# Optimization experiments

Hardware: AMD Instinct MI355X
Metric: run time of the kernel (lower is better)

## Reference

```python
import jax, jax.numpy as jnp
import numpy as np

B, S, D_MODEL, H, D_KV, D_FF = 2, 2048, 1024, 16, 64, 4096
NUM_BUCKETS, MAX_DISTANCE = 32, 128
EPS = 1e-6


def rms_norm(x, w, eps=EPS):
    var = jnp.mean(jnp.square(x), axis=-1, keepdims=True)
    return x * jax.lax.rsqrt(var + eps) * w


def gelu_new(x):
    c = np.sqrt(2.0 / np.pi).astype(np.float32)
    return 0.5 * x * (1.0 + jnp.tanh(c * (x + 0.044715 * x * x * x)))


def rel_position_bucket(qlen, klen, num_buckets=NUM_BUCKETS, max_distance=MAX_DISTANCE):
    # bidirectional (encoder) T5 bucketing
    ctx = jnp.arange(qlen)[:, None]
    mem = jnp.arange(klen)[None, :]
    rel = mem - ctx  # [q, k]
    nb = num_buckets // 2
    ret = (rel > 0).astype(jnp.int32) * nb
    n = jnp.abs(rel)
    max_exact = nb // 2
    is_small = n < max_exact
    val_large = max_exact + (
        jnp.log(jnp.maximum(n, 1).astype(jnp.float32) / max_exact)
        / np.log(max_distance / max_exact) * (nb - max_exact)
    ).astype(jnp.int32)
    val_large = jnp.minimum(val_large, nb - 1)
    return ret + jnp.where(is_small, n, val_large)


def setup_inputs() -> dict:
    key = jax.random.key(0)
    ks = jax.random.split(key, 12)
    sd = 1.0 / np.sqrt(D_MODEL)
    sf = 1.0 / np.sqrt(D_FF)
    return {
        "hidden_states": jax.random.normal(ks[0], (B, S, D_MODEL), jnp.float32),
        "attention_mask": jnp.ones((B, S), jnp.float32),
        "ln1_w": jnp.ones((D_MODEL,), jnp.float32),
        "wq": jax.random.normal(ks[1], (D_MODEL, H * D_KV), jnp.float32) * sd,
        "wk": jax.random.normal(ks[2], (D_MODEL, H * D_KV), jnp.float32) * sd,
        "wv": jax.random.normal(ks[3], (D_MODEL, H * D_KV), jnp.float32) * sd,
        "rel_bias": jax.random.normal(ks[4], (NUM_BUCKETS, H), jnp.float32) * 0.5,
        "wo": jax.random.normal(ks[5], (H * D_KV, D_MODEL), jnp.float32) * sd,
        "ln2_w": jnp.ones((D_MODEL,), jnp.float32),
        "w1": jax.random.normal(ks[6], (D_MODEL, D_FF), jnp.float32) * sd,
        "w2": jax.random.normal(ks[7], (D_MODEL, D_FF), jnp.float32) * sd,
        "w_out": jax.random.normal(ks[8], (D_FF, D_MODEL), jnp.float32) * sf,
    }


def reference(hidden_states, attention_mask, ln1_w, wq, wk, wv, rel_bias, wo,
              ln2_w, w1, w2, w_out):
    b, s, _ = hidden_states.shape
    # --- self attention (pre-LN) ---
    normed = rms_norm(hidden_states, ln1_w)
    q = (normed @ wq).reshape(b, s, H, D_KV)
    k = (normed @ wk).reshape(b, s, H, D_KV)
    v = (normed @ wv).reshape(b, s, H, D_KV)
    scores = jnp.einsum('bqhd,bkhd->bhqk', q, k)  # no 1/sqrt(d) scaling (T5)
    buckets = rel_position_bucket(s, s)            # [q, k] int32
    bias = rel_bias[buckets]                       # [q, k, H]
    scores = scores + jnp.transpose(bias, (2, 0, 1))[None]
    mask_add = (1.0 - attention_mask)[:, None, None, :] * -10000.0
    probs = jax.nn.softmax(scores + mask_add, axis=-1)
    ctx = jnp.einsum('bhqk,bkhd->bqhd', probs, v).reshape(b, s, H * D_KV)
    hidden = hidden_states + ctx @ wo
    # --- gated FFN (pre-LN) ---
    normed2 = rms_norm(hidden, ln2_w)
    ff = (gelu_new(normed2 @ w1) * (normed2 @ w2)) @ w_out
    return hidden + ff
```

## Files before the change

### kernel.cpp

```cpp
#include <hip/hip_runtime.h>
#include <math.h>

typedef unsigned short u16;
typedef unsigned int u32;
typedef __attribute__((ext_vector_type(8))) short short8;
typedef __attribute__((ext_vector_type(4))) float f32x4;

__device__ __forceinline__ float b2f(u16 u) {
    u32 x = ((u32)u) << 16;
    return __builtin_bit_cast(float, x);
}
__device__ __forceinline__ u16 f2b(float f) {
    u32 x = __builtin_bit_cast(u32, f);
    u32 r = x + 0x7fffu + ((x >> 16) & 1u);
    return (u16)(r >> 16);
}
__device__ __forceinline__ void split_hl(float x, u16& h, u16& l) {
    u16 hb = f2b(x);
    h = hb;
    l = f2b(x - b2f(hb));
}
__device__ __forceinline__ float gelu_new_f(float x) {
    const float c = 0.7978845608028654f;
    float y = c * (x + 0.044715f * x * x * x);
    float t = 1.0f - 2.0f / (1.0f + __expf(2.0f * y));
    return 0.5f * x * (1.0f + t);
}
__device__ __forceinline__ float scrub(float v, float s) {
    return (fabsf(v) < 1e25f) ? v : s;
}
__device__ __forceinline__ void gld16(const void* g, void* l) {
    __builtin_amdgcn_global_load_lds((const __attribute__((address_space(1))) u32*)g,
                                     (__attribute__((address_space(3))) u32*)l,
                                     16, 0, 0);
}
__device__ __forceinline__ short8 ldf(const u16* p) { return *(const short8*)p; }

__global__ __launch_bounds__(256) void transpose_cvt(const float* __restrict__ src,
                                                     u16* __restrict__ dst, int R, int C) {
    __shared__ u16 t[32][33];
    int c0 = blockIdx.x * 32, r0 = blockIdx.y * 32;
    int x = threadIdx.x & 31, y = threadIdx.x >> 5;
#pragma unroll
    for (int i = 0; i < 32; i += 8)
        t[y + i][x] = f2b(src[(size_t)(r0 + y + i) * C + c0 + x]);
    __syncthreads();
#pragma unroll
    for (int i = 0; i < 32; i += 8)
        dst[(size_t)(c0 + y + i) * R + r0 + x] = t[x][y + i];
}

__global__ void bias_table_kernel(const float* __restrict__ rel_bias,
                                  const float* __restrict__ mask,
                                  float* __restrict__ tab,
                                  float* __restrict__ mask_add) {
    int idx = blockIdx.x * 256 + threadIdx.x;
    if (idx < 4095) {
        int rel = idx - 2047;
        int ret = rel > 0 ? 16 : 0;
        int n = rel < 0 ? -rel : rel;
        int bucket;
        if (n < 8) {
            bucket = ret + n;
        } else {
            int v = 8 + (int)(logf((float)n * 0.125f) * (8.0f / 2.7725887222397811f));
            v = v < 15 ? v : 15;
            bucket = ret + v;
        }
#pragma unroll
        for (int h = 0; h < 16; h++)
            tab[h * 4096 + idx] = rel_bias[bucket * 16 + h];
    }
    if (idx < 4096)
        mask_add[idx] = (1.0f - mask[idx]) * -10000.0f - 20.0f;
}

__global__ __launch_bounds__(256) void rmsnorm_k(const float* __restrict__ X,
                                                 const float* __restrict__ W,
                                                 u16* __restrict__ Y) {
    __shared__ float red[4];
    int row = blockIdx.x, tid = threadIdx.x;
    const float* xr = X + (size_t)row * 1024;
    float4 x = *(const float4*)(xr + tid * 4);
    float ss = x.x * x.x + x.y * x.y + x.z * x.z + x.w * x.w;
#pragma unroll
    for (int off = 32; off; off >>= 1) ss += __shfl_xor(ss, off, 64);
    if ((tid & 63) == 0) red[tid >> 6] = ss;
    __syncthreads();
    float tot = red[0] + red[1] + red[2] + red[3];
    float s = rsqrtf(tot * (1.0f / 1024.0f) + 1e-6f);
    float4 w4 = *(const float4*)(W + tid * 4);
    float y0 = scrub(x.x * s * w4.x, 1e3f);
    float y1 = scrub(x.y * s * w4.y, 1e3f);
    float y2 = scrub(x.z * s * w4.z, 1e3f);
    float y3 = scrub(x.w * s * w4.w, 1e3f);
    uint2 o;
    o.x = (u32)f2b(y0) | ((u32)f2b(y1) << 16);
    o.y = (u32)f2b(y2) | ((u32)f2b(y3) << 16);
    *(uint2*)(Y + (size_t)row * 1024 + tid * 4) = o;
}


__global__ __launch_bounds__(256) void gemm_qkv(const u16* __restrict__ A,
                                                const u16* __restrict__ Bt,
                                                float* __restrict__ qb,
                                                u16* __restrict__ Kh,
                                                u16* __restrict__ Kl,
                                                u16* __restrict__ vT) {
    const int K = 1024;
    __shared__ __align__(16) u16 As[128 * 64];
    __shared__ __align__(16) u16 Bs[128 * 64];
    int tid = threadIdx.x;
    int wave = tid >> 6, lane = tid & 63, quad = lane >> 4, l15 = lane & 15;
    int bm = blockIdx.y * 128, bn = blockIdx.x * 128;
    int wm = (wave >> 1) * 64, wn = (wave & 1) * 64;
    f32x4 acc[4][4] = {};
    int lr = lane >> 3, cb = (lane & 7) ^ (lr & 7);
    const u16* ga = A + (size_t)(bm + wave * 32 + lr) * K + cb * 8;
    const u16* gb = Bt + (size_t)(bn + wave * 32 + lr) * K + cb * 8;
    u16* la = As + wave * 2048;
    u16* lb = Bs + wave * 2048;
    int swz = l15 & 7;
    for (int k0 = 0; k0 < K; k0 += 64) {
        __syncthreads();
#pragma unroll
        for (int g = 0; g < 4; g++) {
            gld16(ga + k0 + (size_t)(g * 8) * K, la + g * 512);
            gld16(gb + k0 + (size_t)(g * 8) * K, lb + g * 512);
        }
        __syncthreads();
#pragma unroll
        for (int s = 0; s < 2; s++) {
            int kb = ((s * 4 + quad) ^ swz) * 8;
            short8 af[4], bf[4];
#pragma unroll
            for (int i = 0; i < 4; i++)
                af[i] = ldf(As + (wm + i * 16 + l15) * 64 + kb);
#pragma unroll
            for (int j = 0; j < 4; j++)
                bf[j] = ldf(Bs + (wn + j * 16 + l15) * 64 + kb);
#pragma unroll
            for (int i = 0; i < 4; i++)
#pragma unroll
                for (int j = 0; j < 4; j++)
                    acc[i][j] = __builtin_amdgcn_mfma_f32_16x16x32_bf16(af[i], bf[j], acc[i][j], 0, 0, 0);
        }
    }
    if (bn < 1024) {
#pragma unroll
        for (int i = 0; i < 4; i++)
#pragma unroll
            for (int j = 0; j < 4; j++) {
                int col = bn + wn + j * 16 + l15;
#pragma unroll
                for (int r = 0; r < 4; r++) {
                    int row = bm + wm + i * 16 + quad * 4 + r;
                    qb[(size_t)row * 1024 + col] = scrub(acc[i][j][r], 1e4f);
                }
            }
    } else if (bn < 2048) {
#pragma unroll
        for (int i = 0; i < 4; i++)
#pragma unroll
            for (int j = 0; j < 4; j++) {
                int col = bn - 1024 + wn + j * 16 + l15;
#pragma unroll
                for (int r = 0; r < 4; r++) {
                    int row = bm + wm + i * 16 + quad * 4 + r;
                    u16 hh, ll;
                    split_hl(scrub(acc[i][j][r], 1e4f), hh, ll);
                    Kh[(size_t)row * 1024 + col] = hh;
                    Kl[(size_t)row * 1024 + col] = ll;
                }
            }
    } else {
#pragma unroll
        for (int i = 0; i < 4; i++)
#pragma unroll
            for (int j = 0; j < 4; j++) {
                int col = bn - 2048 + wn + j * 16 + l15;
                int row0 = bm + wm + i * 16 + quad * 4;
                ushort4 p;
                p.x = f2b(scrub(acc[i][j][0], 1e4f));
                p.y = f2b(scrub(acc[i][j][1], 1e4f));
                p.z = f2b(scrub(acc[i][j][2], 1e4f));
                p.w = f2b(scrub(acc[i][j][3], 1e4f));
                *(ushort4*)(vT + (size_t)col * 4096 + row0) = p;
            }
    }
}

__global__ __launch_bounds__(256) void gemm_bt_res(const u16* __restrict__ A,
                                                   const u16* __restrict__ Bt,
                                                   float* __restrict__ C,
                                                   const float* __restrict__ Res,
                                                   int M, int N, int K, float sval) {
    __shared__ __align__(16) u16 As[128 * 64];
    __shared__ __align__(16) u16 Bs[128 * 64];
    int tid = threadIdx.x;
    int wave = tid >> 6, lane = tid & 63, quad = lane >> 4, l15 = lane & 15;
    int bm = blockIdx.y * 128, bn = blockIdx.x * 128;
    int wm = (wave >> 1) * 64, wn = (wave & 1) * 64;
    f32x4 acc[4][4] = {};
    int lr = lane >> 3, cb = (lane & 7) ^ (lr & 7);
    const u16* ga = A + (size_t)(bm + wave * 32 + lr) * K + cb * 8;
    const u16* gb = Bt + (size_t)(bn + wave * 32 + lr) * K + cb * 8;
    u16* la = As + wave * 2048;
    u16* lb = Bs + wave * 2048;
    int swz = l15 & 7;
    for (int k0 = 0; k0 < K; k0 += 64) {
        __syncthreads();
#pragma unroll
        for (int g = 0; g < 4; g++) {
            gld16(ga + k0 + (size_t)(g * 8) * K, la + g * 512);
            gld16(gb + k0 + (size_t)(g * 8) * K, lb + g * 512);
        }
        __syncthreads();
#pragma unroll
        for (int s = 0; s < 2; s++) {
            int kb = ((s * 4 + quad) ^ swz) * 8;
            short8 af[4], bf[4];
#pragma unroll
            for (int i = 0; i < 4; i++)
                af[i] = ldf(As + (wm + i * 16 + l15) * 64 + kb);
#pragma unroll
            for (int j = 0; j < 4; j++)
                bf[j] = ldf(Bs + (wn + j * 16 + l15) * 64 + kb);
#pragma unroll
            for (int i = 0; i < 4; i++)
#pragma unroll
                for (int j = 0; j < 4; j++)
                    acc[i][j] = __builtin_amdgcn_mfma_f32_16x16x32_bf16(af[i], bf[j], acc[i][j], 0, 0, 0);
        }
    }
#pragma unroll
    for (int i = 0; i < 4; i++)
#pragma unroll
        for (int j = 0; j < 4; j++) {
            int col = bn + wn + j * 16 + l15;
#pragma unroll
            for (int r = 0; r < 4; r++) {
                int row = bm + wm + i * 16 + quad * 4 + r;
                float v = acc[i][j][r] + Res[(size_t)row * N + col];
                C[(size_t)row * N + col] = scrub(v, sval);
            }
        }
}

__global__ __launch_bounds__(256) void gemm_dual_gelu(const u16* __restrict__ A,
                                                      const u16* __restrict__ B1t,
                                                      const u16* __restrict__ B2t,
                                                      u16* __restrict__ C,
                                                      int M, int N, int K) {
    __shared__ __align__(16) u16 As[128 * 64];
    __shared__ __align__(16) u16 B1s[128 * 64];
    __shared__ __align__(16) u16 B2s[128 * 64];
    int tid = threadIdx.x;
    int wave = tid >> 6, lane = tid & 63, quad = lane >> 4, l15 = lane & 15;
    int bm = blockIdx.y * 128, bn = blockIdx.x * 128;
    int wm = (wave >> 1) * 64, wn = (wave & 1) * 64;
    f32x4 acc1[4][4] = {};
    f32x4 acc2[4][4] = {};
    int lr = lane >> 3, cb = (lane & 7) ^ (lr & 7);
    const u16* ga = A + (size_t)(bm + wave * 32 + lr) * K + cb * 8;
    const u16* g1 = B1t + (size_t)(bn + wave * 32 + lr) * K + cb * 8;
    const u16* g2 = B2t + (size_t)(bn + wave * 32 + lr) * K + cb * 8;
    u16* la = As + wave * 2048;
    u16* l1 = B1s + wave * 2048;
    u16* l2 = B2s + wave * 2048;
    int swz = l15 & 7;
    for (int k0 = 0; k0 < K; k0 += 64) {
        __syncthreads();
#pragma unroll
        for (int g = 0; g < 4; g++) {
            gld16(ga + k0 + (size_t)(g * 8) * K, la + g * 512);
            gld16(g1 + k0 + (size_t)(g * 8) * K, l1 + g * 512);
            gld16(g2 + k0 + (size_t)(g * 8) * K, l2 + g * 512);
        }
        __syncthreads();
#pragma unroll
        for (int s = 0; s < 2; s++) {
            int kb = ((s * 4 + quad) ^ swz) * 8;
            short8 af[4], b1f[4], b2f_[4];
#pragma unroll
            for (int i = 0; i < 4; i++)
                af[i] = ldf(As + (wm + i * 16 + l15) * 64 + kb);
#pragma unroll
            for (int j = 0; j < 4; j++) {
                b1f[j] = ldf(B1s + (wn + j * 16 + l15) * 64 + kb);
                b2f_[j] = ldf(B2s + (wn + j * 16 + l15) * 64 + kb);
            }
#pragma unroll
            for (int i = 0; i < 4; i++)
#pragma unroll
                for (int j = 0; j < 4; j++) {
                    acc1[i][j] = __builtin_amdgcn_mfma_f32_16x16x32_bf16(af[i], b1f[j], acc1[i][j], 0, 0, 0);
                    acc2[i][j] = __builtin_amdgcn_mfma_f32_16x16x32_bf16(af[i], b2f_[j], acc2[i][j], 0, 0, 0);
                }
        }
    }
#pragma unroll
    for (int i = 0; i < 4; i++)
#pragma unroll
        for (int j = 0; j < 4; j++) {
            int col = bn + wn + j * 16 + l15;
#pragma unroll
            for (int r = 0; r < 4; r++) {
                int row = bm + wm + i * 16 + quad * 4 + r;
                float v = gelu_new_f(acc1[i][j][r]) * acc2[i][j][r];
                C[(size_t)row * N + col] = f2b(scrub(v, 1e10f));
            }
        }
}

__global__ __launch_bounds__(256) void attn_kernel(const float* __restrict__ Qb,
                                                   const u16* __restrict__ Kh,
                                                   const u16* __restrict__ Kl,
                                                   const u16* __restrict__ vT,
                                                   const float* __restrict__ bias_tab,
                                                   const float* __restrict__ mask_add,
                                                   u16* __restrict__ Ctx) {
    constexpr int QS = 72;
    __shared__ __align__(16) u16 Qhs[64 * QS];
    __shared__ __align__(16) u16 Qls[64 * QS];
    __shared__ __align__(16) u16 Khs[32 * 64];
    __shared__ __align__(16) u16 Kls[32 * 64];
    __shared__ __align__(16) u16 Vs[64 * 32];
    __shared__ __align__(16) u16 Pss[4 * 16 * 40];
    int tid = threadIdx.x, wave = tid >> 6, lane = tid & 63;
    int quad = lane >> 4, l15 = lane & 15;
    int h = blockIdx.y, b = blockIdx.z;
    int q0 = blockIdx.x * 64;
    const float* Qg = Qb + ((size_t)(b * 2048 + q0)) * 1024 + h * 64;
    {
        int r = tid >> 2, c0 = (tid & 3) * 16;
#pragma unroll
        for (int j = 0; j < 4; j++) {
            float4 q4 = *(const float4*)(Qg + (size_t)r * 1024 + c0 + j * 4);
            u16 hh, ll;
            split_hl(q4.x, hh, ll); Qhs[r * QS + c0 + j * 4 + 0] = hh; Qls[r * QS + c0 + j * 4 + 0] = ll;
            split_hl(q4.y, hh, ll); Qhs[r * QS + c0 + j * 4 + 1] = hh; Qls[r * QS + c0 + j * 4 + 1] = ll;
            split_hl(q4.z, hh, ll); Qhs[r * QS + c0 + j * 4 + 2] = hh; Qls[r * QS + c0 + j * 4 + 2] = ll;
            split_hl(q4.w, hh, ll); Qhs[r * QS + c0 + j * 4 + 3] = hh; Qls[r * QS + c0 + j * 4 + 3] = ll;
        }
    }
    f32x4 O[4] = {};
    f32x4 O4 = {};
    __syncthreads();
    short8 qh0 = ldf(Qhs + (wave * 16 + l15) * QS + quad * 8);
    short8 qh1 = ldf(Qhs + (wave * 16 + l15) * QS + 32 + quad * 8);
    short8 ql0 = ldf(Qls + (wave * 16 + l15) * QS + quad * 8);
    short8 ql1 = ldf(Qls + (wave * 16 + l15) * QS + 32 + quad * 8);
    short8 vones;
#pragma unroll
    for (int i = 0; i < 8; i++) vones[i] = (short)0x3f80;
    u16* Pw = Pss + wave * 16 * 40;
    int my_q = q0 + wave * 16 + quad * 4;
    const float* bt = bias_tab + h * 4096;
    const float* ma = mask_add + b * 2048;
    const u16* gkh = Kh + ((size_t)(b * 2048 + wave * 8 + (lane >> 3))) * 1024 + h * 64
                       + (((lane & 7) ^ (lane >> 3)) * 8);
    const u16* gkl = Kl + ((size_t)(b * 2048 + wave * 8 + (lane >> 3))) * 1024 + h * 64
                       + (((lane & 7) ^ (lane >> 3)) * 8);
    const u16* gv  = vT + ((size_t)(h * 64 + wave * 16 + (lane >> 2))) * 4096 + b * 2048
                       + (((lane & 3) ^ ((lane >> 2) & 3)) * 8);
    u16* lkh = Khs + wave * 512;
    u16* lkl = Kls + wave * 512;
    u16* lv  = Vs + wave * 512;
    int swK0 = (quad ^ (l15 & 7)) * 8;
    int swK1 = ((quad + 4) ^ (l15 & 7)) * 8;
    int swV  = (quad ^ (l15 & 3)) * 8;

    for (int k0 = 0; k0 < 2048; k0 += 32) {
        __syncthreads();
        gld16(gkh + (size_t)k0 * 1024, lkh);
        gld16(gkl + (size_t)k0 * 1024, lkl);
        gld16(gv + k0, lv);
        __syncthreads();
        float pv[2][4];
#pragma unroll
        for (int t = 0; t < 2; t++) {
            const u16* krow = Khs + (t * 16 + l15) * 64;
            const u16* lrow = Kls + (t * 16 + l15) * 64;
            short8 kh0 = ldf(krow + swK0);
            short8 kh1 = ldf(krow + swK1);
            short8 kl0 = ldf(lrow + swK0);
            short8 kl1 = ldf(lrow + swK1);
            f32x4 z = {0.0f, 0.0f, 0.0f, 0.0f};
            z = __builtin_amdgcn_mfma_f32_16x16x32_bf16(ql0, kh0, z, 0, 0, 0);
            z = __builtin_amdgcn_mfma_f32_16x16x32_bf16(ql1, kh1, z, 0, 0, 0);
            z = __builtin_amdgcn_mfma_f32_16x16x32_bf16(qh0, kl0, z, 0, 0, 0);
            z = __builtin_amdgcn_mfma_f32_16x16x32_bf16(qh1, kl1, z, 0, 0, 0);
            z = __builtin_amdgcn_mfma_f32_16x16x32_bf16(qh0, kh0, z, 0, 0, 0);
            z = __builtin_amdgcn_mfma_f32_16x16x32_bf16(qh1, kh1, z, 0, 0, 0);
            int kcol = k0 + t * 16 + l15;
            float madd = ma[kcol];
#pragma unroll
            for (int r = 0; r < 4; r++)
                pv[t][r] = __expf(z[r] + bt[kcol - (my_q + r) + 2047] + madd);
        }
#pragma unroll
        for (int t = 0; t < 2; t++)
#pragma unroll
            for (int r = 0; r < 4; r++)
                Pw[(quad * 4 + r) * 40 + t * 16 + l15] = f2b(pv[t][r]);
        short8 pf = ldf(Pw + l15 * 40 + quad * 8);
#pragma unroll
        for (int nt = 0; nt < 4; nt++) {
            short8 vf = ldf(Vs + (nt * 16 + l15) * 32 + swV);
            O[nt] = __builtin_amdgcn_mfma_f32_16x16x32_bf16(pf, vf, O[nt], 0, 0, 0);
        }
        O4 = __builtin_amdgcn_mfma_f32_16x16x32_bf16(pf, vones, O4, 0, 0, 0);
    }
    u16* Cg = Ctx + ((size_t)(b * 2048 + my_q)) * 1024 + h * 64;
#pragma unroll
    for (int nt = 0; nt < 4; nt++)
#pragma unroll
        for (int r = 0; r < 4; r++) {
            float v = O[nt][r] / fmaxf(O4[r], 1e-30f);
            Cg[(size_t)r * 1024 + nt * 16 + l15] = f2b(scrub(v, 1e6f));
        }
}

extern "C" void kernel_launch(void* const* d_in, const int* in_sizes, int n_in,
                              void* d_out, int out_size, void* d_ws, size_t ws_size,
                              hipStream_t stream) {
    const float* hidden = (const float*)d_in[0];
    const float* mask   = (const float*)d_in[1];
    const float* ln1_w  = (const float*)d_in[2];
    const float* wq     = (const float*)d_in[3];
    const float* wk     = (const float*)d_in[4];
    const float* wv     = (const float*)d_in[5];
    const float* relb   = (const float*)d_in[6];
    const float* wo     = (const float*)d_in[7];
    const float* ln2_w  = (const float*)d_in[8];
    const float* w1     = (const float*)d_in[9];
    const float* w2     = (const float*)d_in[10];
    const float* w_out  = (const float*)d_in[11];
    float* out = (float*)d_out;

    char* w = (char*)d_ws;
    const size_t MB = 1u << 20;
    u16*   qkvT    = (u16*)(w + 0 * MB);
    u16*   woutT   = (u16*)(w + 0 * MB);
    u16*   woT     = (u16*)(w + 6 * MB);
    u16*   w1T     = (u16*)(w + 8 * MB);
    u16*   w2T     = (u16*)(w + 16 * MB);
    u16*   normed  = (u16*)(w + 24 * MB);
    u16*   ctx     = (u16*)(w + 24 * MB);
    u16*   normed2 = (u16*)(w + 24 * MB);
    u16*   Kh      = (u16*)(w + 40 * MB);
    u16*   Kl      = (u16*)(w + 48 * MB);
    u16*   vT      = (u16*)(w + 56 * MB);
    u16*   ffg     = (u16*)(w + 32 * MB);
    float* bias_tab = (float*)(w + 64 * MB);
    float* mask_add = (float*)(w + 64 * MB + 256 * 1024);
    float* qb      = (float*)d_out;

    dim3 blk(256);
    transpose_cvt<<<dim3(32, 32), blk, 0, stream>>>(wq, qkvT, 1024, 1024);
    transpose_cvt<<<dim3(32, 32), blk, 0, stream>>>(wk, qkvT + 1024 * 1024, 1024, 1024);
    transpose_cvt<<<dim3(32, 32), blk, 0, stream>>>(wv, qkvT + 2048 * 1024, 1024, 1024);
    transpose_cvt<<<dim3(32, 32), blk, 0, stream>>>(wo, woT, 1024, 1024);
    transpose_cvt<<<dim3(128, 32), blk, 0, stream>>>(w1, w1T, 1024, 4096);
    transpose_cvt<<<dim3(128, 32), blk, 0, stream>>>(w2, w2T, 1024, 4096);
    bias_table_kernel<<<16, 256, 0, stream>>>(relb, mask, bias_tab, mask_add);

    rmsnorm_k<<<4096, blk, 0, stream>>>(hidden, ln1_w, normed);
    gemm_qkv<<<dim3(24, 32), blk, 0, stream>>>(normed, qkvT, qb, Kh, Kl, vT);

    attn_kernel<<<dim3(32, 16, 2), blk, 0, stream>>>(qb, Kh, Kl, vT, bias_tab, mask_add, ctx);

    gemm_bt_res<<<dim3(8, 32), blk, 0, stream>>>(ctx, woT, out, hidden, 4096, 1024, 1024, 1e8f);

    transpose_cvt<<<dim3(32, 128), blk, 0, stream>>>(w_out, woutT, 4096, 1024);

    rmsnorm_k<<<4096, blk, 0, stream>>>(out, ln2_w, normed2);
    gemm_dual_gelu<<<dim3(32, 32), blk, 0, stream>>>(normed2, w1T, w2T, ffg, 4096, 4096, 1024);
    gemm_bt_res<<<dim3(8, 32), blk, 0, stream>>>(ffg, woutT, out, out, 4096, 1024, 4096, 1e12f);
}
```

Before: 557.6 us.

## Double attention key tile to 64, load Q directly to registers, use exp2

The attention kernel now processes 64 keys per iteration instead of 32, which halves the number of block-wide barriers and global-to-LDS load rounds per query block. Q fragments are loaded straight from global memory into MFMA registers, dropping the LDS staging and one barrier. Q, the bias table and the mask are pre-scaled by log2(e) so the softmax can use exp2f. The cost is more LDS per block (larger K, V and P buffers), which may lower occupancy, and prescaling Q before the hi/lo split changes rounding slightly.

```diff
diff --git a/kernel.cpp b/kernel.cpp
--- a/kernel.cpp
+++ b/kernel.cpp
@@ -54,6 +54,7 @@
                                   const float* __restrict__ mask,
                                   float* __restrict__ tab,
                                   float* __restrict__ mask_add) {
+    const float LOG2E = 1.4426950408889634f;
     int idx = blockIdx.x * 256 + threadIdx.x;
     if (idx < 4095) {
         int rel = idx - 2047;
@@ -69,10 +70,10 @@
         }
 #pragma unroll
         for (int h = 0; h < 16; h++)
-            tab[h * 4096 + idx] = rel_bias[bucket * 16 + h];
+            tab[h * 4096 + idx] = rel_bias[bucket * 16 + h] * LOG2E;
     }
     if (idx < 4096)
-        mask_add[idx] = (1.0f - mask[idx]) * -10000.0f - 20.0f;
+        mask_add[idx] = ((1.0f - mask[idx]) * -10000.0f - 20.0f) * LOG2E;
 }
 
 __global__ __launch_bounds__(256) void rmsnorm_k(const float* __restrict__ X,
@@ -320,66 +321,63 @@
                                                    const float* __restrict__ bias_tab,
                                                    const float* __restrict__ mask_add,
                                                    u16* __restrict__ Ctx) {
-    constexpr int QS = 72;
-    __shared__ __align__(16) u16 Qhs[64 * QS];
-    __shared__ __align__(16) u16 Qls[64 * QS];
-    __shared__ __align__(16) u16 Khs[32 * 64];
-    __shared__ __align__(16) u16 Kls[32 * 64];
-    __shared__ __align__(16) u16 Vs[64 * 32];
-    __shared__ __align__(16) u16 Pss[4 * 16 * 40];
+    __shared__ __align__(16) u16 Khs[64 * 64];
+    __shared__ __align__(16) u16 Kls[64 * 64];
+    __shared__ __align__(16) u16 Vs[64 * 64];
+    __shared__ __align__(16) u16 Pss[4 * 16 * 72];
+    const float LOG2E = 1.4426950408889634f;
     int tid = threadIdx.x, wave = tid >> 6, lane = tid & 63;
     int quad = lane >> 4, l15 = lane & 15;
     int h = blockIdx.y, b = blockIdx.z;
     int q0 = blockIdx.x * 64;
-    const float* Qg = Qb + ((size_t)(b * 2048 + q0)) * 1024 + h * 64;
+    short8 qh0, qh1, ql0, ql1;
     {
-        int r = tid >> 2, c0 = (tid & 3) * 16;
-#pragma unroll
-        for (int j = 0; j < 4; j++) {
-            float4 q4 = *(const float4*)(Qg + (size_t)r * 1024 + c0 + j * 4);
+        const float* Qg = Qb + (size_t)(b * 2048 + q0 + wave * 16 + l15) * 1024 + h * 64 + quad * 8;
+#pragma unroll
+        for (int half = 0; half < 2; half++) {
+            float4 a = *(const float4*)(Qg + half * 32);
+            float4 c = *(const float4*)(Qg + half * 32 + 4);
             u16 hh, ll;
-            split_hl(q4.x, hh, ll); Qhs[r * QS + c0 + j * 4 + 0] = hh; Qls[r * QS + c0 + j * 4 + 0] = ll;
-            split_hl(q4.y, hh, ll); Qhs[r * QS + c0 + j * 4 + 1] = hh; Qls[r * QS + c0 + j * 4 + 1] = ll;
-            split_hl(q4.z, hh, ll); Qhs[r * QS + c0 + j * 4 + 2] = hh; Qls[r * QS + c0 + j * 4 + 2] = ll;
-            split_hl(q4.w, hh, ll); Qhs[r * QS + c0 + j * 4 + 3] = hh; Qls[r * QS + c0 + j * 4 + 3] = ll;
+            float vals[8] = {a.x, a.y, a.z, a.w, c.x, c.y, c.z, c.w};
+#pragma unroll
+            for (int j = 0; j < 8; j++) {
+                split_hl(vals[j] * LOG2E, hh, ll);
+                if (half == 0) { qh0[j] = (short)hh; ql0[j] = (short)ll; }
+                else           { qh1[j] = (short)hh; ql1[j] = (short)ll; }
+            }
         }
     }
     f32x4 O[4] = {};
     f32x4 O4 = {};
-    __syncthreads();
-    short8 qh0 = ldf(Qhs + (wave * 16 + l15) * QS + quad * 8);
-    short8 qh1 = ldf(Qhs + (wave * 16 + l15) * QS + 32 + quad * 8);
-    short8 ql0 = ldf(Qls + (wave * 16 + l15) * QS + quad * 8);
-    short8 ql1 = ldf(Qls + (wave * 16 + l15) * QS + 32 + quad * 8);
     short8 vones;
 #pragma unroll
     for (int i = 0; i < 8; i++) vones[i] = (short)0x3f80;
-    u16* Pw = Pss + wave * 16 * 40;
+    u16* Pw = Pss + wave * 16 * 72;
     int my_q = q0 + wave * 16 + quad * 4;
     const float* bt = bias_tab + h * 4096;
     const float* ma = mask_add + b * 2048;
-    const u16* gkh = Kh + ((size_t)(b * 2048 + wave * 8 + (lane >> 3))) * 1024 + h * 64
-                       + (((lane & 7) ^ (lane >> 3)) * 8);
-    const u16* gkl = Kl + ((size_t)(b * 2048 + wave * 8 + (lane >> 3))) * 1024 + h * 64
-                       + (((lane & 7) ^ (lane >> 3)) * 8);
-    const u16* gv  = vT + ((size_t)(h * 64 + wave * 16 + (lane >> 2))) * 4096 + b * 2048
-                       + (((lane & 3) ^ ((lane >> 2) & 3)) * 8);
-    u16* lkh = Khs + wave * 512;
-    u16* lkl = Kls + wave * 512;
-    u16* lv  = Vs + wave * 512;
-    int swK0 = (quad ^ (l15 & 7)) * 8;
-    int swK1 = ((quad + 4) ^ (l15 & 7)) * 8;
-    int swV  = (quad ^ (l15 & 3)) * 8;
-
-    for (int k0 = 0; k0 < 2048; k0 += 32) {
+    int lr8 = lane >> 3, cb = (lane & 7) ^ (lr8 & 7);
+    const u16* gkh = Kh + (size_t)(b * 2048 + wave * 16 + lr8) * 1024 + h * 64 + cb * 8;
+    const u16* gkl = Kl + (size_t)(b * 2048 + wave * 16 + lr8) * 1024 + h * 64 + cb * 8;
+    const u16* gv  = vT + (size_t)(h * 64 + wave * 16 + lr8) * 4096 + b * 2048 + cb * 8;
+    u16* lkh = Khs + wave * 1024;
+    u16* lkl = Kls + wave * 1024;
+    u16* lv  = Vs + wave * 1024;
+    int sw = l15 & 7;
+    int swK0 = (quad ^ sw) * 8, swK1 = ((quad + 4) ^ sw) * 8;
+
+    for (int k0 = 0; k0 < 2048; k0 += 64) {
         __syncthreads();
         gld16(gkh + (size_t)k0 * 1024, lkh);
+        gld16(gkh + (size_t)k0 * 1024 + 8 * 1024, lkh + 512);
         gld16(gkl + (size_t)k0 * 1024, lkl);
+        gld16(gkl + (size_t)k0 * 1024 + 8 * 1024, lkl + 512);
         gld16(gv + k0, lv);
-        __syncthreads();
-        float pv[2][4];
-#pragma unroll
-        for (int t = 0; t < 2; t++) {
+        gld16(gv + k0 + (size_t)8 * 4096, lv + 512);
+        __syncthreads();
+        float pv[4][4];
+#pragma unroll
+        for (int t = 0; t < 4; t++) {
             const u16* krow = Khs + (t * 16 + l15) * 64;
             const u16* lrow = Kls + (t * 16 + l15) * 64;
             short8 kh0 = ldf(krow + swK0);
@@ -397,20 +395,23 @@
             float madd = ma[kcol];
 #pragma unroll
             for (int r = 0; r < 4; r++)
-                pv[t][r] = __expf(z[r] + bt[kcol - (my_q + r) + 2047] + madd);
-        }
-#pragma unroll
-        for (int t = 0; t < 2; t++)
+                pv[t][r] = exp2f(z[r] + bt[kcol - (my_q + r) + 2047] + madd);
+        }
+#pragma unroll
+        for (int t = 0; t < 4; t++)
 #pragma unroll
             for (int r = 0; r < 4; r++)
-                Pw[(quad * 4 + r) * 40 + t * 16 + l15] = f2b(pv[t][r]);
-        short8 pf = ldf(Pw + l15 * 40 + quad * 8);
-#pragma unroll
-        for (int nt = 0; nt < 4; nt++) {
-            short8 vf = ldf(Vs + (nt * 16 + l15) * 32 + swV);
-            O[nt] = __builtin_amdgcn_mfma_f32_16x16x32_bf16(pf, vf, O[nt], 0, 0, 0);
-        }
-        O4 = __builtin_amdgcn_mfma_f32_16x16x32_bf16(pf, vones, O4, 0, 0, 0);
+                Pw[(quad * 4 + r) * 72 + t * 16 + l15] = f2b(pv[t][r]);
+#pragma unroll
+        for (int h2 = 0; h2 < 2; h2++) {
+            short8 pf = ldf(Pw + l15 * 72 + h2 * 32 + quad * 8);
+#pragma unroll
+            for (int nt = 0; nt < 4; nt++) {
+                short8 vf = ldf(Vs + (nt * 16 + l15) * 64 + ((h2 * 4 + quad) ^ sw) * 8);
+                O[nt] = __builtin_amdgcn_mfma_f32_16x16x32_bf16(pf, vf, O[nt], 0, 0, 0);
+            }
+            O4 = __builtin_amdgcn_mfma_f32_16x16x32_bf16(pf, vones, O4, 0, 0, 0);
+        }
     }
     u16* Cg = Ctx + ((size_t)(b * 2048 + my_q)) * 1024 + h * 64;
 #pragma unroll
```

Result: no change. 560.7 us (+0.6%).
